# Performance work log

Hardware: AMD Instinct MI355X
Metric: run time of the kernel (lower is better)

## Reference

```python
import jax, jax.numpy as jnp
import numpy as np

N_HEAD = 8


def build_mask(T, N):
    """Boolean mask [L, L], True = blocked. Mirrors the torch st_mask construction
    for text_mask_mode='part_only', text_to_motion_attn=False, all domains present."""
    L = 3 * T + 5 * N
    motion = 3 * T
    m = np.zeros((L, L), dtype=bool)
    # motion x motion: start fully blocked, then carve block-causal structure
    m[:motion, :motion] = True
    causal = np.tril(np.ones((T, T), dtype=bool))          # incl. diagonal
    strict = np.tril(np.ones((T, T), dtype=bool), k=-1)    # strictly lower
    m[0:T, 0:T] = ~causal
    m[T:2*T, 0:T] = ~causal
    m[T:2*T, T:2*T] = ~strict
    m[T:2*T, 2*T:3*T] = ~strict
    m[2*T:3*T, 0:T] = ~causal
    m[2*T:3*T, T:2*T] = ~causal
    m[2*T:3*T, 2*T:3*T] = ~strict
    # motion queries cannot see text keys
    m[:motion, motion:] = True
    # text queries cannot see motion keys (text_to_motion_attn=False)
    m[motion:, :motion] = True
    # part_only: upper-body rows see upper/torso/whole/simple_tag text domains;
    # lower-body rows see lower/torso/whole/simple_tag text domains
    ts = motion
    up, down = slice(T, 2*T), slice(2*T, 3*T)
    for d in (0, 2, 3, 4):
        m[up, ts + d*N: ts + (d+1)*N] = False
    for d in (1, 2, 3, 4):
        m[down, ts + d*N: ts + (d+1)*N] = False
    # text x text region stays all-False (full attention among text tokens)
    return jnp.asarray(m)


def setup_inputs() -> dict:
    key = jax.random.key(0)
    ks = jax.random.split(key, 9)
    B, T_motion, N, C = 2, 1024, 64, 512
    L = 3 * T_motion + 5 * N
    s = 1.0 / np.sqrt(C)
    return {
        "x": jax.random.normal(ks[0], (B, L, C), dtype=jnp.float32),
        "Wq": jax.random.normal(ks[1], (C, C), dtype=jnp.float32) * s,
        "bq": jnp.zeros((C,), dtype=jnp.float32),
        "Wk": jax.random.normal(ks[2], (C, C), dtype=jnp.float32) * s,
        "bk": jnp.zeros((C,), dtype=jnp.float32),
        "Wv": jax.random.normal(ks[3], (C, C), dtype=jnp.float32) * s,
        "bv": jnp.zeros((C,), dtype=jnp.float32),
        "Wp": jax.random.normal(ks[4], (C, C), dtype=jnp.float32) * s,
        "bp": jnp.zeros((C,), dtype=jnp.float32),
        "T_motion": T_motion,
        "N": N,
    }


def reference(x, Wq, bq, Wk, bk, Wv, bv, Wp, bp, T_motion, N):
    B, L, C = x.shape
    H = N_HEAD
    dh = C // H
    mask = build_mask(int(T_motion), int(N))  # [L, L] bool, True = blocked

    def split_heads(t):  # [B, L, C] -> [B, H, L, dh]
        return t.reshape(B, L, H, dh).transpose(0, 2, 1, 3)

    q = split_heads(x @ Wq + bq)
    k = split_heads(x @ Wk + bk)
    v = split_heads(x @ Wv + bv)

    att = jnp.einsum("bhqd,bhkd->bhqk", q, k) * (1.0 / np.sqrt(dh))
    att = jnp.where(mask[None, None], -jnp.inf, att)
    att = jax.nn.softmax(att, axis=-1)
    y = jnp.einsum("bhqk,bhkd->bhqd", att, v)
    y = y.transpose(0, 2, 1, 3).reshape(B, L, C)
    return y @ Wp + bp
```

## Files before the change

### kernel.cpp

```cpp
#include <hip/hip_runtime.h>
#include <hip/hip_bf16.h>
#include <math.h>

typedef __attribute__((ext_vector_type(8))) short bf16x8;
typedef __attribute__((ext_vector_type(4))) short short4v;
typedef __attribute__((ext_vector_type(4))) float f32x4;
typedef __attribute__((ext_vector_type(2))) unsigned int u32x2;

#define DEVI __device__ __forceinline__

constexpr int Bb  = 2;
constexpr int Tm  = 1024;
constexpr int Ntx = 64;
constexpr int Hh  = 8;
constexpr int Ll  = 3*Tm + 5*Ntx;
constexpr int Mm  = Bb*Ll;
constexpr int MOT = 3*Tm;
constexpr int UPH = 75;
constexpr int PST = 72;

DEVI short f2b(float f) {
  unsigned u = __builtin_bit_cast(unsigned, f);
  u = u + 0x7fffu + ((u >> 16) & 1u);
  return (short)(u >> 16);
}

DEVI void gld16(const void* g, void* l) {
  __builtin_amdgcn_global_load_lds(
      (const __attribute__((address_space(1))) unsigned*)g,
      (__attribute__((address_space(3))) unsigned*)l, 16, 0, 0);
}

DEVI f32x4 mfma16(bf16x8 a, bf16x8 b, f32x4 c) {
  return __builtin_amdgcn_mfma_f32_16x16x32_bf16(a, b, c, 0, 0, 0);
}


__global__ __launch_bounds__(256) void cast_x_kern(const float* __restrict__ x,
                                                   short* __restrict__ xb) {
  int i = (blockIdx.x*256 + threadIdx.x)*4;
  float4 v = *(const float4*)(x + i);
  short4v r;
  r.x = f2b(v.x); r.y = f2b(v.y); r.z = f2b(v.z); r.w = f2b(v.w);
  *(short4v*)(xb + i) = r;
}

__global__ __launch_bounds__(256) void prep_w_kern(
    const float* __restrict__ Wq, const float* __restrict__ Wk,
    const float* __restrict__ Wv, const float* __restrict__ Wp,
    short* __restrict__ WtQKV, short* __restrict__ WpT) {
  int idx = blockIdx.x*256 + threadIdx.x;
  int mat = idx >> 18;
  int n = (idx >> 9) & 511;
  int k = idx & 511;
  const float* W = (mat == 0) ? Wq : (mat == 1) ? Wk : (mat == 2) ? Wv : Wp;
  short s = f2b(W[k*512 + n]);
  if (mat < 3) WtQKV[((size_t)(mat*512 + n))*512 + k] = s;
  else         WpT[(size_t)n*512 + k] = s;
}


template<int MODE>
__global__ __launch_bounds__(256) void gemm_bt(
    const short* __restrict__ A, const short* __restrict__ Bt,
    const float* __restrict__ bias_q, const float* __restrict__ bias_k,
    const float* __restrict__ bias_v,
    short* __restrict__ Qb, short* __restrict__ Kb, short* __restrict__ Vt,
    float* __restrict__ outf) {
  __shared__ __align__(16) short At[128*32];
  __shared__ __align__(16) short Bs[128*32];
  const int tid = threadIdx.x;
  const int w = tid >> 6, lane = tid & 63;
  const int col = lane & 15, g = lane >> 4;
  const int tm = blockIdx.x, tn = blockIdx.y;
  const int wm = w >> 1, wn = w & 1;

  f32x4 acc[4][4] = {};

  for (int k0 = 0; k0 < 512; k0 += 32) {
    __syncthreads();
#pragma unroll
    for (int it = 0; it < 2; ++it) {
      int e0 = w*512 + it*2048 + lane*8;
      int row = e0 >> 5, cc = e0 & 31;
      gld16(A  + (size_t)(tm*128 + row)*512 + k0 + cc, At + w*512 + it*2048);
      gld16(Bt + (size_t)(tn*128 + row)*512 + k0 + cc, Bs + w*512 + it*2048);
    }
    __syncthreads();
    bf16x8 af[4], bfr[4];
#pragma unroll
    for (int i = 0; i < 4; ++i)
      af[i] = *(const bf16x8*)(At + (wm*64 + i*16 + col)*32 + g*8);
#pragma unroll
    for (int j = 0; j < 4; ++j)
      bfr[j] = *(const bf16x8*)(Bs + (wn*64 + j*16 + col)*32 + g*8);
#pragma unroll
    for (int i = 0; i < 4; ++i)
#pragma unroll
      for (int j = 0; j < 4; ++j)
        acc[i][j] = mfma16(af[i], bfr[j], acc[i][j]);
  }

#pragma unroll
  for (int i = 0; i < 4; ++i) {
    int mbase = tm*128 + wm*64 + i*16 + g*4;
#pragma unroll
    for (int j = 0; j < 4; ++j) {
      int ncol = tn*128 + wn*64 + j*16 + col;
#pragma unroll
      for (int r = 0; r < 4; ++r) {
        int mrow = mbase + r;
        float v = acc[i][j][r];
        if constexpr (MODE == 0) {
          float bias = (ncol < 512) ? bias_q[ncol]
                     : (ncol < 1024) ? bias_k[ncol - 512] : bias_v[ncol - 1024];
          v += bias;
          int bb = (mrow >= Ll) ? 1 : 0;
          int lpos = mrow - bb*Ll;
          int nn = ncol & 511;
          int h = nn >> 6, dd = nn & 63;
          int bh = bb*8 + h;
          if (ncol < 512) {
            Qb[((size_t)(bh*Ll + lpos))*64 + dd] = f2b(v*0.18033688f);
          } else if (ncol < 1024) {
            Kb[((size_t)(bh*Ll + lpos))*64 + dd] = f2b(v);
          } else {
            Vt[((size_t)(bh*64 + dd))*Ll + lpos] = f2b(v);
          }
        } else {
          outf[(size_t)mrow*512 + ncol] = v + bias_q[ncol];
        }
      }
    }
  }
}


__global__ __launch_bounds__(256) void attn_kern(
    const short* __restrict__ Qb, const short* __restrict__ Kb,
    const short* __restrict__ Vt, float* __restrict__ slots,
    short* __restrict__ attout) {
  __shared__ __align__(16) short Kls[2][4096];
  __shared__ __align__(16) short Vls[2][4096];
  __shared__ __align__(16) short Pls[4][32*PST];
  const int tid = threadIdx.x;
  const int w = tid >> 6, lane = tid & 63;
  const int col = lane & 15, g = lane >> 4;

  const int v  = (blockIdx.x & 7)*150 + (blockIdx.x >> 3);
  const int bh = v / UPH;
  const int lr = v - bh*UPH;

  int qsec, seg = 0, j = 0, t3 = 0;
  if (lr < 56) {
    int jj = lr/7, s = lr - jj*7;
    j = 7 - jj;
    if (s == 0)      qsec = 0;
    else if (s <= 3) { qsec = 1; seg = s - 1; }
    else             { qsec = 2; seg = s - 4; }
  } else if (lr < 72) {
    int t = lr - 56; qsec = 1 + (t & 1); j = t >> 1; seg = 3;
  } else { qsec = 3; t3 = lr - 72; }

  const int q0b = (qsec < 3) ? qsec*Tm + j*128 : MOT + ((t3 == 2) ? 192 : t3*128);
  const int t0w = j*128 + w*32;
  const int q0w = q0b + w*32;

  int kbase = 0, off = 0, nb;
  bool masked;
  if (qsec == 3)      { kbase = MOT;  nb = 5;       masked = false; }
  else if (qsec == 0) { kbase = 0;    nb = 2*j + 2; masked = true; off = 0; }
  else if (seg == 0)  { kbase = 0;    nb = 2*j + 2; masked = true; off = 0; }
  else if (seg == 1)  { kbase = Tm;   nb = 2*j + 2; masked = true; off = (qsec == 1) ? 1 : 0; }
  else if (seg == 2)  { kbase = 2*Tm; nb = 2*j + 2; masked = true; off = 1; }
  else                { kbase = 0;    nb = 4;       masked = false; }

  auto keyof = [&](int i) -> int {
    if (qsec == 3) return MOT + i*64;
    if (!masked) { int d = (i == 0) ? ((qsec == 1) ? 0 : 1) : i + 1; return MOT + d*64; }
    return kbase + i*64;
  };

  const short* Kbase_ = Kb + (size_t)bh*Ll*64;
  const short* Vbase_ = Vt + (size_t)bh*64*Ll;

  bf16x8 aq[2][2];
#pragma unroll
  for (int qf = 0; qf < 2; ++qf) {
    const short* p = Qb + ((size_t)bh*Ll + q0w + qf*16 + col)*64;
    aq[qf][0] = *(const bf16x8*)(p + g*8);
    aq[qf][1] = *(const bf16x8*)(p + 32 + g*8);
  }
  const int qv[2] = { t0w + col, t0w + 16 + col };

  float ls[2] = {0.f, 0.f};
  f32x4 out[2][4] = {};

  auto stage = [&](int buf, int key0) {
#pragma unroll
    for (int it = 0; it < 2; ++it) {
      int L = it*4096 + tid*16;
      int row = L >> 7;
      int sw = (row & 7) << 4;
      gld16((const char*)Kbase_ + (size_t)key0*128 + (L ^ sw),
            (char*)&Kls[buf][0] + it*4096 + w*1024);
      gld16((const char*)(Vbase_ + (size_t)row*Ll + key0) + ((L & 127) ^ sw),
            (char*)&Vls[buf][0] + it*4096 + w*1024);
    }
  };

  auto compute = [&](int buf, int i) {
    const int swc = (col & 7) << 4;
    f32x4 s[2][4];
#pragma unroll
    for (int kk = 0; kk < 4; ++kk) {
      const char* base = (const char*)&Kls[buf][0] + (kk*16 + col)*128;
      bf16x8 k0 = *(const bf16x8*)(base + ((g*16) ^ swc));
      bf16x8 k1 = *(const bf16x8*)(base + ((64 + g*16) ^ swc));
#pragma unroll
      for (int qf = 0; qf < 2; ++qf) {
        f32x4 t = {0,0,0,0};
        t = mfma16(k0, aq[qf][0], t);
        t = mfma16(k1, aq[qf][1], t);
        s[qf][kk] = t;
      }
    }
    const bool dm = masked && (i*64 + 63 + off > t0w);
    const int kl = i*64 + off + g*4;
    short* pw = &Pls[w][0];
#pragma unroll
    for (int qf = 0; qf < 2; ++qf) {
      float lsl = 0.f;
#pragma unroll
      for (int kk = 0; kk < 4; ++kk) {
        float pe[4];
#pragma unroll
        for (int r = 0; r < 4; ++r) {
          float p = __builtin_amdgcn_exp2f(s[qf][kk][r]);
          if (dm && (kl + kk*16 + r > qv[qf])) p = 0.f;
          pe[r] = p; lsl += p;
        }
        unsigned pk0, pk1;
        asm("v_cvt_pk_bf16_f32 %0, %1, %2" : "=v"(pk0) : "v"(pe[0]), "v"(pe[1]));
        asm("v_cvt_pk_bf16_f32 %0, %1, %2" : "=v"(pk1) : "v"(pe[2]), "v"(pe[3]));
        u32x2 pk; pk.x = pk0; pk.y = pk1;
        *(u32x2*)(pw + (qf*16 + col)*PST + kk*16 + g*4) = pk;
      }
      ls[qf] += lsl;
    }
    bf16x8 pa[2][2];
#pragma unroll
    for (int qf = 0; qf < 2; ++qf) {
      const short* base2 = &Pls[w][0] + (qf*16 + col)*PST;
      pa[qf][0] = *(const bf16x8*)(base2 + g*8);
      pa[qf][1] = *(const bf16x8*)(base2 + 32 + g*8);
    }
#pragma unroll
    for (int ch = 0; ch < 4; ++ch) {
      const char* base = (const char*)&Vls[buf][0] + (ch*16 + col)*128;
      bf16x8 v0 = *(const bf16x8*)(base + ((g*16) ^ swc));
      bf16x8 v1 = *(const bf16x8*)(base + ((64 + g*16) ^ swc));
#pragma unroll
      for (int qf = 0; qf < 2; ++qf) {
        out[qf][ch] = mfma16(pa[qf][0], v0, out[qf][ch]);
        out[qf][ch] = mfma16(pa[qf][1], v1, out[qf][ch]);
      }
    }
  };

  stage(0, keyof(0));
  for (int i = 0; i < nb; ++i) {
    if (i + 1 < nb) {
      stage((i + 1) & 1, keyof(i + 1));
      asm volatile("s_waitcnt vmcnt(4)" ::: "memory");
    } else {
      asm volatile("s_waitcnt vmcnt(0)" ::: "memory");
    }
    __builtin_amdgcn_sched_barrier(0);
    __builtin_amdgcn_s_barrier();
    bool skip = masked && (t0w + 31 < i*64 + off);
    if (!skip) compute(i & 1, i);
    __builtin_amdgcn_s_barrier();
  }

  float rs[2];
#pragma unroll
  for (int qf = 0; qf < 2; ++qf) {
    float t = ls[qf];
    t += __shfl_xor(t, 16);
    t += __shfl_xor(t, 32);
    rs[qf] = t;
  }

  if (qsec == 1 || qsec == 2) {
    float* sp = slots + ((((size_t)bh*2 + (qsec - 1))*8 + j)*4 + seg)*8320;
#pragma unroll
    for (int qf = 0; qf < 2; ++qf) {
#pragma unroll
      for (int ch = 0; ch < 4; ++ch)
#pragma unroll
        for (int r = 0; r < 4; ++r)
          sp[(w*32 + qf*16 + g*4 + r)*64 + ch*16 + col] = out[qf][ch][r];
      if (g == 0)
        sp[8192 + w*32 + qf*16 + col] = rs[qf];
    }
  } else {
    const int b = bh >> 3, h = bh & 7;
#pragma unroll
    for (int qf = 0; qf < 2; ++qf)
#pragma unroll
      for (int r = 0; r < 4; ++r) {
        float dv = __shfl(rs[qf], g*4 + r);
        float inv = 1.0f / dv;
        size_t rowoff = ((size_t)(b*Ll + q0w + qf*16 + g*4 + r))*512 + h*64;
#pragma unroll
        for (int ch = 0; ch < 4; ++ch)
          attout[rowoff + ch*16 + col] = f2b(out[qf][ch][r]*inv);
      }
  }
}

__global__ __launch_bounds__(256) void fin_kern(const float* __restrict__ slots,
                                                short* __restrict__ attout) {
  const int w = threadIdx.x >> 6, lane = threadIdx.x & 63;
  const int ridx = blockIdx.x*4 + w;
  const int bh = ridx >> 11;
  const int rr = ridx & 2047;
  const int qsec = 1 + (rr >> 10);
  const int rl = rr & 1023;
  const int j = rl >> 7;
  const int row_local = rl & 127;
  const float* base = slots + (((size_t)bh*2 + (qsec - 1))*8 + j)*4*8320;
  float a = 0.f, l = 0.f;
#pragma unroll
  for (int s = 0; s < 4; ++s) {
    a += base[s*8320 + row_local*64 + lane];
    l += base[s*8320 + 8192 + row_local];
  }
  const int b = bh >> 3, h = bh & 7;
  attout[((size_t)(b*Ll + qsec*Tm + rl))*512 + h*64 + lane] = f2b(a / l);
}


extern "C" void kernel_launch(void* const* d_in, const int* in_sizes, int n_in,
                              void* d_out, int out_size, void* d_ws, size_t ws_size,
                              hipStream_t stream) {
  const float* x  = (const float*)d_in[0];
  const float* Wq = (const float*)d_in[1];
  const float* bq = (const float*)d_in[2];
  const float* Wk = (const float*)d_in[3];
  const float* bk = (const float*)d_in[4];
  const float* Wv = (const float*)d_in[5];
  const float* bv = (const float*)d_in[6];
  const float* Wp = (const float*)d_in[7];
  const float* bp = (const float*)d_in[8];
  float* out = (float*)d_out;

  short* ws = (short*)d_ws;
  constexpr size_t SZ  = (size_t)Mm*512;
  short* xb    = ws;
  short* WtQKV = xb + SZ;
  short* WpT   = WtQKV + (size_t)1536*512;
  short* Qb    = WpT + (size_t)512*512;
  short* Kb    = Qb + SZ;
  short* Vt    = Kb + SZ;
  short* att   = Vt + SZ;
  float* slots = (float*)(att + SZ);

  cast_x_kern<<<dim3(Mm*512/1024), dim3(256), 0, stream>>>(x, xb);
  prep_w_kern<<<dim3(4096), dim3(256), 0, stream>>>(Wq, Wk, Wv, Wp, WtQKV, WpT);
  gemm_bt<0><<<dim3(53, 12), dim3(256), 0, stream>>>(xb, WtQKV, bq, bk, bv,
                                                     Qb, Kb, Vt, nullptr);
  attn_kern<<<dim3(1200), dim3(256), 0, stream>>>(Qb, Kb, Vt, slots, att);
  fin_kern<<<dim3(8192), dim3(256), 0, stream>>>(slots, att);
  gemm_bt<1><<<dim3(53, 4), dim3(256), 0, stream>>>(att, WpT, bp, nullptr, nullptr,
                                                    nullptr, nullptr, nullptr, out);
}
```

Measured before the change: 101.5 us.

## Merge prep kernels and switch attention staging to register-prefetched single LDS buffer

```diff
diff --git a/kernel.cpp b/kernel.cpp
--- a/kernel.cpp
+++ b/kernel.cpp
@@ -36,27 +36,27 @@
 }
 
 
-__global__ __launch_bounds__(256) void cast_x_kern(const float* __restrict__ x,
-                                                   short* __restrict__ xb) {
-  int i = (blockIdx.x*256 + threadIdx.x)*4;
-  float4 v = *(const float4*)(x + i);
-  short4v r;
-  r.x = f2b(v.x); r.y = f2b(v.y); r.z = f2b(v.z); r.w = f2b(v.w);
-  *(short4v*)(xb + i) = r;
-}
-
-__global__ __launch_bounds__(256) void prep_w_kern(
+__global__ __launch_bounds__(256) void prep_kern(
+    const float* __restrict__ x,  short* __restrict__ xb,
     const float* __restrict__ Wq, const float* __restrict__ Wk,
     const float* __restrict__ Wv, const float* __restrict__ Wp,
     short* __restrict__ WtQKV, short* __restrict__ WpT) {
-  int idx = blockIdx.x*256 + threadIdx.x;
-  int mat = idx >> 18;
-  int n = (idx >> 9) & 511;
-  int k = idx & 511;
-  const float* W = (mat == 0) ? Wq : (mat == 1) ? Wk : (mat == 2) ? Wv : Wp;
-  short s = f2b(W[k*512 + n]);
-  if (mat < 3) WtQKV[((size_t)(mat*512 + n))*512 + k] = s;
-  else         WpT[(size_t)n*512 + k] = s;
+  if (blockIdx.x < 3392) {
+    int i = (blockIdx.x*256 + threadIdx.x)*4;
+    float4 v = *(const float4*)(x + i);
+    short4v r;
+    r.x = f2b(v.x); r.y = f2b(v.y); r.z = f2b(v.z); r.w = f2b(v.w);
+    *(short4v*)(xb + i) = r;
+  } else {
+    int idx = (blockIdx.x - 3392)*256 + threadIdx.x;
+    int mat = idx >> 18;
+    int n = (idx >> 9) & 511;
+    int k = idx & 511;
+    const float* W = (mat == 0) ? Wq : (mat == 1) ? Wk : (mat == 2) ? Wv : Wp;
+    short s = f2b(W[k*512 + n]);
+    if (mat < 3) WtQKV[((size_t)(mat*512 + n))*512 + k] = s;
+    else         WpT[(size_t)n*512 + k] = s;
+  }
 }
 
 
@@ -136,12 +136,12 @@
 }
 
 
-__global__ __launch_bounds__(256) void attn_kern(
+__global__ __launch_bounds__(256, 4) void attn_kern(
     const short* __restrict__ Qb, const short* __restrict__ Kb,
     const short* __restrict__ Vt, float* __restrict__ slots,
     short* __restrict__ attout) {
-  __shared__ __align__(16) short Kls[2][4096];
-  __shared__ __align__(16) short Vls[2][4096];
+  __shared__ __align__(16) short Kls[4096];
+  __shared__ __align__(16) short Vls[4096];
   __shared__ __align__(16) short Pls[4][32*PST];
   const int tid = threadIdx.x;
   const int w = tid >> 6, lane = tid & 63;
@@ -196,25 +196,32 @@
   float ls[2] = {0.f, 0.f};
   f32x4 out[2][4] = {};
 
-  auto stage = [&](int buf, int key0) {
+  int4 kreg[2], vreg[2];
+  auto loadregs = [&](int key0) {
 #pragma unroll
     for (int it = 0; it < 2; ++it) {
       int L = it*4096 + tid*16;
       int row = L >> 7;
-      int sw = (row & 7) << 4;
-      gld16((const char*)Kbase_ + (size_t)key0*128 + (L ^ sw),
-            (char*)&Kls[buf][0] + it*4096 + w*1024);
-      gld16((const char*)(Vbase_ + (size_t)row*Ll + key0) + ((L & 127) ^ sw),
-            (char*)&Vls[buf][0] + it*4096 + w*1024);
+      kreg[it] = *(const int4*)((const char*)Kbase_ + (size_t)key0*128 + L);
+      vreg[it] = *(const int4*)((const char*)(Vbase_ + (size_t)row*Ll + key0) + (L & 127));
     }
   };
-
-  auto compute = [&](int buf, int i) {
+  auto writelds = [&]() {
+#pragma unroll
+    for (int it = 0; it < 2; ++it) {
+      int L = it*4096 + tid*16;
+      int sw = ((L >> 7) & 7) << 4;
+      *(int4*)((char*)Kls + (L ^ sw)) = kreg[it];
+      *(int4*)((char*)Vls + (L ^ sw)) = vreg[it];
+    }
+  };
+
+  auto compute = [&](int i) {
     const int swc = (col & 7) << 4;
     f32x4 s[2][4];
 #pragma unroll
     for (int kk = 0; kk < 4; ++kk) {
-      const char* base = (const char*)&Kls[buf][0] + (kk*16 + col)*128;
+      const char* base = (const char*)Kls + (kk*16 + col)*128;
       bf16x8 k0 = *(const bf16x8*)(base + ((g*16) ^ swc));
       bf16x8 k1 = *(const bf16x8*)(base + ((64 + g*16) ^ swc));
 #pragma unroll
@@ -257,7 +264,7 @@
     }
 #pragma unroll
     for (int ch = 0; ch < 4; ++ch) {
-      const char* base = (const char*)&Vls[buf][0] + (ch*16 + col)*128;
+      const char* base = (const char*)Vls + (ch*16 + col)*128;
       bf16x8 v0 = *(const bf16x8*)(base + ((g*16) ^ swc));
       bf16x8 v1 = *(const bf16x8*)(base + ((64 + g*16) ^ swc));
 #pragma unroll
@@ -268,19 +275,20 @@
     }
   };
 
-  stage(0, keyof(0));
+  loadregs(keyof(0));
+  asm volatile("s_waitcnt vmcnt(0)" ::: "memory");
+  writelds();
+  __builtin_amdgcn_s_barrier();
   for (int i = 0; i < nb; ++i) {
+    if (i + 1 < nb) loadregs(keyof(i + 1));
+    bool skip = masked && (t0w + 31 < i*64 + off);
+    if (!skip) compute(i);
+    __builtin_amdgcn_s_barrier();
     if (i + 1 < nb) {
-      stage((i + 1) & 1, keyof(i + 1));
-      asm volatile("s_waitcnt vmcnt(4)" ::: "memory");
-    } else {
       asm volatile("s_waitcnt vmcnt(0)" ::: "memory");
-    }
-    __builtin_amdgcn_sched_barrier(0);
-    __builtin_amdgcn_s_barrier();
-    bool skip = masked && (t0w + 31 < i*64 + off);
-    if (!skip) compute(i & 1, i);
-    __builtin_amdgcn_s_barrier();
+      writelds();
+      __builtin_amdgcn_s_barrier();
+    }
   }
 
   float rs[2];
@@ -367,8 +375,8 @@
   short* att   = Vt + SZ;
   float* slots = (float*)(att + SZ);
 
-  cast_x_kern<<<dim3(Mm*512/1024), dim3(256), 0, stream>>>(x, xb);
-  prep_w_kern<<<dim3(4096), dim3(256), 0, stream>>>(Wq, Wk, Wv, Wp, WtQKV, WpT);
+  prep_kern<<<dim3(3392 + 4096), dim3(256), 0, stream>>>(x, xb, Wq, Wk, Wv, Wp,
+                                                         WtQKV, WpT);
   gemm_bt<0><<<dim3(53, 12), dim3(256), 0, stream>>>(xb, WtQKV, bq, bk, bv,
                                                      Qb, Kb, Vt, nullptr);
   attn_kern<<<dim3(1200), dim3(256), 0, stream>>>(Qb, Kb, Vt, slots, att);
```

Measured after the change: 120.9 us. 1.19x slower.
